# Optimization experiments

Hardware: AMD Instinct MI355X
Metric: run time of the kernel (lower is better)

The kernel has to match this reference:

```python
import jax, jax.numpy as jnp
import numpy as np

N_NODES = 40000
N_EDGES = 640000
IN_CH, HID_CH, OUT_CH = 128, 128, 64
NEG_SLOPE = 0.2  # PyG GATConv default


def _add_self_loops(src, dst, n):
    loop = jnp.arange(n, dtype=src.dtype)
    return jnp.concatenate([src, loop]), jnp.concatenate([dst, loop])


def gcn_conv(x, src, dst, W, b, n):
    # PyG GCNConv: add self-loops, symmetric degree norm, then aggregate.
    h = x @ W                                   # [N, F_out]
    s, d = _add_self_loops(src, dst, n)
    deg = jax.ops.segment_sum(jnp.ones_like(d, dtype=h.dtype), d, num_segments=n)
    dinv = jnp.where(deg > 0, jax.lax.rsqrt(deg), 0.0)
    norm = dinv[s] * dinv[d]                    # [E+N]
    msg = h[s] * norm[:, None]                  # gather + scale
    out = jax.ops.segment_sum(msg, d, num_segments=n)
    return out + b


def gat_conv(x, src, dst, W, a_src, a_dst, b, n):
    # PyG GATConv, heads=1: self-loops, edge-wise LeakyReLU attention logits,
    # softmax over incoming edges per dst node, weighted scatter-add.
    h = x @ W                                   # [N, F_out]
    s, d = _add_self_loops(src, dst, n)
    logit = jax.nn.leaky_relu((h @ a_src)[s] + (h @ a_dst)[d], NEG_SLOPE)  # [E+N]
    mx = jax.ops.segment_max(logit, d, num_segments=n)
    e = jnp.exp(logit - mx[d])
    z = jax.ops.segment_sum(e, d, num_segments=n)
    alpha = e / z[d]
    out = jax.ops.segment_sum(h[s] * alpha[:, None], d, num_segments=n)
    return out + b


def setup_inputs() -> dict:
    key = jax.random.key(0)
    ks = jax.random.split(key, 16)
    x = jax.random.normal(ks[0], (N_NODES, IN_CH), dtype=jnp.float32)
    edge_index = jax.random.randint(ks[1], (2, N_EDGES), 0, N_NODES, dtype=jnp.int64 if jax.config.jax_enable_x64 else jnp.int32)
    glorot = lambda k, fi, fo: jax.random.normal(k, (fi, fo), jnp.float32) * np.sqrt(2.0 / (fi + fo))
    params = {
        'W1': glorot(ks[2], IN_CH, HID_CH),   'b1': jnp.zeros((HID_CH,), jnp.float32),
        'Wg1': glorot(ks[3], HID_CH, HID_CH), 'ag1_src': jax.random.normal(ks[4], (HID_CH,), jnp.float32) * 0.1,
        'ag1_dst': jax.random.normal(ks[5], (HID_CH,), jnp.float32) * 0.1, 'bg1': jnp.zeros((HID_CH,), jnp.float32),
        'W2': glorot(ks[6], HID_CH, OUT_CH),  'b2': jnp.zeros((OUT_CH,), jnp.float32),
        'Wg2': glorot(ks[7], OUT_CH, OUT_CH), 'ag2_src': jax.random.normal(ks[8], (OUT_CH,), jnp.float32) * 0.1,
        'ag2_dst': jax.random.normal(ks[9], (OUT_CH,), jnp.float32) * 0.1, 'bg2': jnp.zeros((OUT_CH,), jnp.float32),
    }
    return {'x': x, 'edge_index': edge_index, **params}


def reference(x, edge_index, W1, b1, Wg1, ag1_src, ag1_dst, bg1, W2, b2, Wg2, ag2_src, ag2_dst, bg2):
    n = x.shape[0]
    src, dst = edge_index[0], edge_index[1]
    h = jax.nn.relu(gcn_conv(x, src, dst, W1, b1, n))
    # dropout(p=0.5) is identity in eval mode
    encoded = gat_conv(h, src, dst, Wg1, ag1_src, ag1_dst, bg1, n)
    h = jax.nn.relu(gcn_conv(encoded, src, dst, W2, b2, n))
    decoded = gat_conv(h, src, dst, Wg2, ag2_src, ag2_dst, bg2, n)
    return encoded, decoded
```

## Files before the change

### kernel.cpp

```cpp
#include <hip/hip_runtime.h>

#define NN 40000
#define NE 640000
#define NSB ((NN + 255) / 256)

typedef unsigned int uint32;

static __device__ __forceinline__ float lrelu(float x) { return x > 0.0f ? x : 0.2f * x; }

static __device__ __forceinline__ float wave_max(float v) {
    for (int off = 32; off; off >>= 1) v = fmaxf(v, __shfl_xor(v, off));
    return v;
}
static __device__ __forceinline__ float wave_sum(float v) {
    for (int off = 32; off; off >>= 1) v += __shfl_xor(v, off);
    return v;
}

static __device__ __forceinline__ uint32 bfr(float x) {
    uint32 u = __float_as_uint(x);
    return u + 0x7FFFu + ((u >> 16) & 1u);
}
static __device__ __forceinline__ uint32 pack2(float a, float b) {
    return (bfr(a) >> 16) | (bfr(b) & 0xFFFF0000u);
}
static __device__ __forceinline__ float lo16(uint32 v) { return __uint_as_float(v << 16); }
static __device__ __forceinline__ float hi16(uint32 v) { return __uint_as_float(v & 0xFFFF0000u); }

template <int FIN, int FOUT>
__global__ __launch_bounds__(256) void k_gemm_t(const float* __restrict__ X,
                                                const float* __restrict__ W,
                                                float* __restrict__ Y,
                                                uint32* __restrict__ Y16) {
    constexpr int XLD = FIN + 4;
    __shared__ float ws[FIN * 64];
    __shared__ float xs[64 * XLD];
    const int t = threadIdx.x;
    const int row0 = blockIdx.x * 64;
    const int col0 = blockIdx.y * 64;

    for (int i = t; i < FIN * 16; i += 256) {
        int k = i >> 4, cc = (i & 15) << 2;
        *(float4*)&ws[k * 64 + cc] = *(const float4*)&W[k * FOUT + col0 + cc];
    }
    for (int i = t; i < 64 * (FIN / 4); i += 256) {
        int r = i / (FIN / 4), kk = (i % (FIN / 4)) << 2;
        *(float4*)&xs[r * XLD + kk] = *(const float4*)&X[(size_t)(row0 + r) * FIN + kk];
    }
    __syncthreads();

    const int c0 = (t & 15) << 2;
    const int r0 = (t >> 4) << 2;
    float acc[4][4] = {};
#pragma unroll 2
    for (int k = 0; k < FIN; k += 4) {
        float4 xv[4], wv[4];
#pragma unroll
        for (int i = 0; i < 4; ++i) xv[i] = *(const float4*)&xs[(r0 + i) * XLD + k];
#pragma unroll
        for (int j = 0; j < 4; ++j) wv[j] = *(const float4*)&ws[(k + j) * 64 + c0];
#pragma unroll
        for (int i = 0; i < 4; ++i) {
            acc[i][0] = fmaf(xv[i].x, wv[0].x, acc[i][0]);
            acc[i][1] = fmaf(xv[i].x, wv[0].y, acc[i][1]);
            acc[i][2] = fmaf(xv[i].x, wv[0].z, acc[i][2]);
            acc[i][3] = fmaf(xv[i].x, wv[0].w, acc[i][3]);
            acc[i][0] = fmaf(xv[i].y, wv[1].x, acc[i][0]);
            acc[i][1] = fmaf(xv[i].y, wv[1].y, acc[i][1]);
            acc[i][2] = fmaf(xv[i].y, wv[1].z, acc[i][2]);
            acc[i][3] = fmaf(xv[i].y, wv[1].w, acc[i][3]);
            acc[i][0] = fmaf(xv[i].z, wv[2].x, acc[i][0]);
            acc[i][1] = fmaf(xv[i].z, wv[2].y, acc[i][1]);
            acc[i][2] = fmaf(xv[i].z, wv[2].z, acc[i][2]);
            acc[i][3] = fmaf(xv[i].z, wv[2].w, acc[i][3]);
            acc[i][0] = fmaf(xv[i].w, wv[3].x, acc[i][0]);
            acc[i][1] = fmaf(xv[i].w, wv[3].y, acc[i][1]);
            acc[i][2] = fmaf(xv[i].w, wv[3].z, acc[i][2]);
            acc[i][3] = fmaf(xv[i].w, wv[3].w, acc[i][3]);
        }
    }
#pragma unroll
    for (int i = 0; i < 4; ++i) {
        float4 v = make_float4(acc[i][0], acc[i][1], acc[i][2], acc[i][3]);
        size_t base = (size_t)(row0 + r0 + i) * FOUT + col0 + c0;
        *(float4*)&Y[base] = v;
        uint2 p = make_uint2(pack2(v.x, v.y), pack2(v.z, v.w));
        *(uint2*)&Y16[base >> 1] = p;
    }
}

__global__ void k_zero_int(int* __restrict__ p, int n) {
    int i = blockIdx.x * blockDim.x + threadIdx.x;
    if (i < n) p[i] = 0;
}
__global__ void k_count(const int* __restrict__ dst, int* __restrict__ cnt) {
    int e = blockIdx.x * blockDim.x + threadIdx.x;
    if (e < NE) atomicAdd(&cnt[dst[e]], 1);
}
__global__ void k_bsum(const int* __restrict__ cnt, int* __restrict__ bsum) {
    __shared__ int wsums[4];
    int i = blockIdx.x * 256 + threadIdx.x;
    int v = (i < NN) ? cnt[i] : 0;
    for (int off = 32; off; off >>= 1) v += __shfl_down(v, off);
    if ((threadIdx.x & 63) == 0) wsums[threadIdx.x >> 6] = v;
    __syncthreads();
    if (threadIdx.x == 0) bsum[blockIdx.x] = wsums[0] + wsums[1] + wsums[2] + wsums[3];
}
__global__ void k_scanpart(const int* __restrict__ bsum, int* __restrict__ bofs,
                           int* __restrict__ rowptr) {
    __shared__ int s[256];
    int t = threadIdx.x;
    int v = (t < NSB) ? bsum[t] : 0;
    s[t] = v;
    __syncthreads();
    for (int off = 1; off < 256; off <<= 1) {
        int u = (t >= off) ? s[t - off] : 0;
        __syncthreads();
        s[t] += u;
        __syncthreads();
    }
    if (t < NSB) bofs[t] = s[t] - v;
    if (t == 0) rowptr[NN] = NE;
}
__global__ void k_scatter(const int* __restrict__ cnt, const int* __restrict__ bofs,
                          int* __restrict__ rowptr, int* __restrict__ cursor) {
    __shared__ int wsums[4];
    int t = threadIdx.x;
    int lane = t & 63, w = t >> 6;
    int i = blockIdx.x * 256 + t;
    int v = (i < NN) ? cnt[i] : 0;
    int x = v;
    for (int off = 1; off < 64; off <<= 1) {
        int u = __shfl_up(x, off);
        if (lane >= off) x += u;
    }
    if (lane == 63) wsums[w] = x;
    __syncthreads();
    int wofs = 0;
    for (int k = 0; k < w; ++k) wofs += wsums[k];
    int excl = bofs[blockIdx.x] + wofs + x - v;
    if (i < NN) {
        rowptr[i] = excl;
        cursor[i] = excl;
    }
}
__global__ void k_fill(const int* __restrict__ src, const int* __restrict__ dst,
                       int* __restrict__ cursor, int* __restrict__ csr_src) {
    int e = blockIdx.x * blockDim.x + threadIdx.x;
    if (e < NE) {
        int p = atomicAdd(&cursor[dst[e]], 1);
        csr_src[p] = src[e];
    }
}
__global__ void k_dinv(const int* __restrict__ rowptr, float* __restrict__ dinv) {
    int i = blockIdx.x * blockDim.x + threadIdx.x;
    if (i < NN) dinv[i] = rsqrtf(1.0f + (float)(rowptr[i + 1] - rowptr[i]));
}

static __device__ __forceinline__ void gath128(const uint32* __restrict__ h16, int lane, int myi,
                                               float myw, int cnt, float* acc) {
    for (int j = 0; j < cnt; j += 8) {
        int s[8];
        float w[8];
#pragma unroll
        for (int u = 0; u < 8; ++u) {
            s[u] = __shfl(myi, j + u);
            w[u] = __shfl(myw, j + u);
        }
        uint32 v[8];
#pragma unroll
        for (int u = 0; u < 8; ++u) v[u] = h16[(size_t)s[u] * 64 + lane];
#pragma unroll
        for (int u = 0; u < 8; ++u) {
            acc[0] = fmaf(w[u], lo16(v[u]), acc[0]);
            acc[1] = fmaf(w[u], hi16(v[u]), acc[1]);
        }
    }
}
static __device__ __forceinline__ void gath64(const uint32* __restrict__ h16, int lane, int myi,
                                              float myw, int cnt, float* acc) {
    int hh = lane >> 5, cl = lane & 31;
    for (int j = 0; j < cnt; j += 16) {
        int s[8];
        float w[8];
#pragma unroll
        for (int u = 0; u < 8; ++u) {
            int e = j + 2 * u + hh;
            s[u] = __shfl(myi, e);
            w[u] = __shfl(myw, e);
        }
        uint32 v[8];
#pragma unroll
        for (int u = 0; u < 8; ++u) v[u] = h16[(size_t)s[u] * 32 + cl];
#pragma unroll
        for (int u = 0; u < 8; ++u) {
            acc[0] = fmaf(w[u], lo16(v[u]), acc[0]);
            acc[1] = fmaf(w[u], hi16(v[u]), acc[1]);
        }
    }
}

template <int F>
__global__ __launch_bounds__(256) void k_gcn_gather_w(const int* __restrict__ rowptr,
                                                      const int* __restrict__ csr_src,
                                                      const uint32* __restrict__ h16,
                                                      const float* __restrict__ dinv,
                                                      const float* __restrict__ b,
                                                      float* __restrict__ out) {
    int node = blockIdx.x * 4 + (threadIdx.x >> 6);
    int lane = threadIdx.x & 63;
    int beg = rowptr[node], end = rowptr[node + 1];
    float dd = dinv[node];
    float acc[2] = {0.0f, 0.0f};

    for (int g = beg; g < end; g += 64) {
        int cnt = end - g;
        if (cnt > 64) cnt = 64;
        int myi = node;
        float myw = 0.0f;
        if (lane < cnt) {
            int s = csr_src[g + lane];
            myi = s;
            myw = dinv[s];
        }
        if (F == 128)
            gath128(h16, lane, myi, myw, cnt, acc);
        else
            gath64(h16, lane, myi, myw, cnt, acc);
    }
    if (F == 128) {
        uint32 sv = h16[(size_t)node * 64 + lane];
        acc[0] = fmaf(dd, lo16(sv), acc[0]);
        acc[1] = fmaf(dd, hi16(sv), acc[1]);
        int c = lane * 2;
        float2 r;
        r.x = fmaxf(fmaf(acc[0], dd, b[c]), 0.0f);
        r.y = fmaxf(fmaf(acc[1], dd, b[c + 1]), 0.0f);
        *(float2*)&out[(size_t)node * 128 + c] = r;
    } else {
        acc[0] += __shfl_xor(acc[0], 32);
        acc[1] += __shfl_xor(acc[1], 32);
        if (lane < 32) {
            uint32 sv = h16[(size_t)node * 32 + lane];
            acc[0] = fmaf(dd, lo16(sv), acc[0]);
            acc[1] = fmaf(dd, hi16(sv), acc[1]);
            int c = lane * 2;
            float2 r;
            r.x = fmaxf(fmaf(acc[0], dd, b[c]), 0.0f);
            r.y = fmaxf(fmaf(acc[1], dd, b[c + 1]), 0.0f);
            *(float2*)&out[(size_t)node * 64 + c] = r;
        }
    }
}

__global__ void k_gat_scalars(const float* __restrict__ hg, const float* __restrict__ a_s,
                              const float* __restrict__ a_d, float* __restrict__ asrc,
                              float* __restrict__ adst, int F) {
    int node = blockIdx.x * (blockDim.x >> 6) + (threadIdx.x >> 6);
    int lane = threadIdx.x & 63;
    if (node >= NN) return;
    float s = 0.0f, d = 0.0f;
    for (int c = lane; c < F; c += 64) {
        float v = hg[(size_t)node * F + c];
        s += v * a_s[c];
        d += v * a_d[c];
    }
    for (int off = 32; off; off >>= 1) {
        s += __shfl_down(s, off);
        d += __shfl_down(d, off);
    }
    if (lane == 0) {
        asrc[node] = s;
        adst[node] = d;
    }
}

template <int F>
__global__ __launch_bounds__(256) void k_gat_gather_w(const int* __restrict__ rowptr,
                                                      const int* __restrict__ csr_src,
                                                      const uint32* __restrict__ h16,
                                                      const float* __restrict__ asrc,
                                                      const float* __restrict__ adst,
                                                      const float* __restrict__ b,
                                                      float* __restrict__ out) {
    int node = blockIdx.x * 4 + (threadIdx.x >> 6);
    int lane = threadIdx.x & 63;
    int beg = rowptr[node], end = rowptr[node + 1];
    int deg = end - beg;
    float ad = adst[node];
    float slog = lrelu(asrc[node] + ad);
    float acc[2] = {0.0f, 0.0f};
    float wself;

    if (deg <= 64) {
        int myi = node;
        float logit = -1e30f;
        if (lane < deg) {
            myi = csr_src[beg + lane];
            logit = lrelu(asrc[myi] + ad);
        }
        float m = fmaxf(slog, wave_max(logit));
        float e = (lane < deg) ? __expf(logit - m) : 0.0f;
        float z = wave_sum(e) + __expf(slog - m);
        float zi = 1.0f / z;
        float myw = e * zi;
        wself = __expf(slog - m) * zi;
        if (F == 128)
            gath128(h16, lane, myi, myw, deg, acc);
        else
            gath64(h16, lane, myi, myw, deg, acc);
    } else {
        float lm = slog;
        for (int j = beg + lane; j < end; j += 64) lm = fmaxf(lm, lrelu(asrc[csr_src[j]] + ad));
        float m = wave_max(lm);
        float lz = 0.0f;
        for (int j = beg + lane; j < end; j += 64)
            lz += __expf(lrelu(asrc[csr_src[j]] + ad) - m);
        float z = wave_sum(lz) + __expf(slog - m);
        float zi = 1.0f / z;
        wself = __expf(slog - m) * zi;
        for (int g = beg; g < end; g += 64) {
            int cnt = end - g;
            if (cnt > 64) cnt = 64;
            int myi = node;
            float myw = 0.0f;
            if (lane < cnt) {
                int s = csr_src[g + lane];
                myi = s;
                myw = __expf(lrelu(asrc[s] + ad) - m) * zi;
            }
            if (F == 128)
                gath128(h16, lane, myi, myw, cnt, acc);
            else
                gath64(h16, lane, myi, myw, cnt, acc);
        }
    }
    if (F == 128) {
        uint32 sv = h16[(size_t)node * 64 + lane];
        acc[0] = fmaf(wself, lo16(sv), acc[0]);
        acc[1] = fmaf(wself, hi16(sv), acc[1]);
        int c = lane * 2;
        float2 r;
        r.x = acc[0] + b[c];
        r.y = acc[1] + b[c + 1];
        *(float2*)&out[(size_t)node * 128 + c] = r;
    } else {
        acc[0] += __shfl_xor(acc[0], 32);
        acc[1] += __shfl_xor(acc[1], 32);
        if (lane < 32) {
            uint32 sv = h16[(size_t)node * 32 + lane];
            acc[0] = fmaf(wself, lo16(sv), acc[0]);
            acc[1] = fmaf(wself, hi16(sv), acc[1]);
            int c = lane * 2;
            float2 r;
            r.x = acc[0] + b[c];
            r.y = acc[1] + b[c + 1];
            *(float2*)&out[(size_t)node * 64 + c] = r;
        }
    }
}

extern "C" void kernel_launch(void* const* d_in, const int* in_sizes, int n_in,
                              void* d_out, int out_size, void* d_ws, size_t ws_size,
                              hipStream_t stream) {
    const float* x = (const float*)d_in[0];
    const int* src = (const int*)d_in[1];
    const int* dst = src + NE;
    const float* W1 = (const float*)d_in[2];
    const float* b1 = (const float*)d_in[3];
    const float* Wg1 = (const float*)d_in[4];
    const float* ag1s = (const float*)d_in[5];
    const float* ag1d = (const float*)d_in[6];
    const float* bg1 = (const float*)d_in[7];
    const float* W2 = (const float*)d_in[8];
    const float* b2 = (const float*)d_in[9];
    const float* Wg2 = (const float*)d_in[10];
    const float* ag2s = (const float*)d_in[11];
    const float* ag2d = (const float*)d_in[12];
    const float* bg2 = (const float*)d_in[13];

    float* enc = (float*)d_out;
    float* dec = enc + (size_t)NN * 128;

    float* ws = (float*)d_ws;
    float* bufA = ws;
    float* bufB = bufA + (size_t)NN * 128;
    uint32* bufA16 = (uint32*)(bufB + (size_t)NN * 128);
    float* dinv = (float*)(bufA16 + (size_t)NN * 64);
    float* asrc = dinv + NN;
    float* adst = asrc + NN;
    int* cnt = (int*)(adst + NN);
    int* rowptr = cnt + NN;
    int* cursor = rowptr + NN + 1;
    int* csr_src = cursor + NN;
    int* bsum = csr_src + NE;
    int* bofs = bsum + NSB;

    const int TB = 256;
    int gN = (NN + TB - 1) / TB;
    int gE = (NE + TB - 1) / TB;
    int gScal = (NN + 3) / 4;
    int gWave = NN / 4;

    k_zero_int<<<gN, TB, 0, stream>>>(cnt, NN);
    k_count<<<gE, TB, 0, stream>>>(dst, cnt);
    k_bsum<<<NSB, 256, 0, stream>>>(cnt, bsum);
    k_scanpart<<<1, 256, 0, stream>>>(bsum, bofs, rowptr);
    k_scatter<<<NSB, 256, 0, stream>>>(cnt, bofs, rowptr, cursor);
    k_fill<<<gE, TB, 0, stream>>>(src, dst, cursor, csr_src);
    k_dinv<<<gN, TB, 0, stream>>>(rowptr, dinv);

    k_gemm_t<128, 128><<<dim3(NN / 64, 2), 256, 0, stream>>>(x, W1, bufA, bufA16);
    k_gcn_gather_w<128><<<gWave, 256, 0, stream>>>(rowptr, csr_src, bufA16, dinv, b1, bufB);

    k_gemm_t<128, 128><<<dim3(NN / 64, 2), 256, 0, stream>>>(bufB, Wg1, bufA, bufA16);
    k_gat_scalars<<<gScal, TB, 0, stream>>>(bufA, ag1s, ag1d, asrc, adst, 128);
    k_gat_gather_w<128><<<gWave, 256, 0, stream>>>(rowptr, csr_src, bufA16, asrc, adst, bg1, enc);

    k_gemm_t<128, 64><<<dim3(NN / 64, 1), 256, 0, stream>>>(enc, W2, bufA, bufA16);
    k_gcn_gather_w<64><<<gWave, 256, 0, stream>>>(rowptr, csr_src, bufA16, dinv, b2, bufB);

    k_gemm_t<64, 64><<<dim3(NN / 64, 1), 256, 0, stream>>>(bufB, Wg2, bufA, bufA16);
    k_gat_scalars<<<gScal, TB, 0, stream>>>(bufA, ag2s, ag2d, asrc, adst, 64);
    k_gat_gather_w<64><<<gWave, 256, 0, stream>>>(rowptr, csr_src, bufA16, asrc, adst, bg2, dec);
}
```

Measured before the change: 264.1 us.

## Use bf16 MFMA GEMMs with bf16 intermediate activations between layers

```diff
diff --git a/kernel.cpp b/kernel.cpp
--- a/kernel.cpp
+++ b/kernel.cpp
@@ -3,8 +3,12 @@
 #define NN 40000
 #define NE 640000
 #define NSB ((NN + 255) / 256)
+#define NNP (NN + 64)
 
 typedef unsigned int uint32;
+typedef unsigned short ushort;
+typedef __attribute__((ext_vector_type(8))) short bf16x8;
+typedef __attribute__((ext_vector_type(4))) float f32x4;
 
 static __device__ __forceinline__ float lrelu(float x) { return x > 0.0f ? x : 0.2f * x; }
 
@@ -21,72 +25,96 @@
     uint32 u = __float_as_uint(x);
     return u + 0x7FFFu + ((u >> 16) & 1u);
 }
+static __device__ __forceinline__ ushort bf16of(float x) { return (ushort)(bfr(x) >> 16); }
 static __device__ __forceinline__ uint32 pack2(float a, float b) {
     return (bfr(a) >> 16) | (bfr(b) & 0xFFFF0000u);
 }
 static __device__ __forceinline__ float lo16(uint32 v) { return __uint_as_float(v << 16); }
 static __device__ __forceinline__ float hi16(uint32 v) { return __uint_as_float(v & 0xFFFF0000u); }
 
-template <int FIN, int FOUT>
-__global__ __launch_bounds__(256) void k_gemm_t(const float* __restrict__ X,
-                                                const float* __restrict__ W,
-                                                float* __restrict__ Y,
-                                                uint32* __restrict__ Y16) {
-    constexpr int XLD = FIN + 4;
-    __shared__ float ws[FIN * 64];
-    __shared__ float xs[64 * XLD];
-    const int t = threadIdx.x;
-    const int row0 = blockIdx.x * 64;
-    const int col0 = blockIdx.y * 64;
-
-    for (int i = t; i < FIN * 16; i += 256) {
-        int k = i >> 4, cc = (i & 15) << 2;
-        *(float4*)&ws[k * 64 + cc] = *(const float4*)&W[k * FOUT + col0 + cc];
-    }
-    for (int i = t; i < 64 * (FIN / 4); i += 256) {
-        int r = i / (FIN / 4), kk = (i % (FIN / 4)) << 2;
-        *(float4*)&xs[r * XLD + kk] = *(const float4*)&X[(size_t)(row0 + r) * FIN + kk];
-    }
-    __syncthreads();
-
-    const int c0 = (t & 15) << 2;
-    const int r0 = (t >> 4) << 2;
-    float acc[4][4] = {};
-#pragma unroll 2
-    for (int k = 0; k < FIN; k += 4) {
-        float4 xv[4], wv[4];
-#pragma unroll
-        for (int i = 0; i < 4; ++i) xv[i] = *(const float4*)&xs[(r0 + i) * XLD + k];
-#pragma unroll
-        for (int j = 0; j < 4; ++j) wv[j] = *(const float4*)&ws[(k + j) * 64 + c0];
-#pragma unroll
-        for (int i = 0; i < 4; ++i) {
-            acc[i][0] = fmaf(xv[i].x, wv[0].x, acc[i][0]);
-            acc[i][1] = fmaf(xv[i].x, wv[0].y, acc[i][1]);
-            acc[i][2] = fmaf(xv[i].x, wv[0].z, acc[i][2]);
-            acc[i][3] = fmaf(xv[i].x, wv[0].w, acc[i][3]);
-            acc[i][0] = fmaf(xv[i].y, wv[1].x, acc[i][0]);
-            acc[i][1] = fmaf(xv[i].y, wv[1].y, acc[i][1]);
-            acc[i][2] = fmaf(xv[i].y, wv[1].z, acc[i][2]);
-            acc[i][3] = fmaf(xv[i].y, wv[1].w, acc[i][3]);
-            acc[i][0] = fmaf(xv[i].z, wv[2].x, acc[i][0]);
-            acc[i][1] = fmaf(xv[i].z, wv[2].y, acc[i][1]);
-            acc[i][2] = fmaf(xv[i].z, wv[2].z, acc[i][2]);
-            acc[i][3] = fmaf(xv[i].z, wv[2].w, acc[i][3]);
-            acc[i][0] = fmaf(xv[i].w, wv[3].x, acc[i][0]);
-            acc[i][1] = fmaf(xv[i].w, wv[3].y, acc[i][1]);
-            acc[i][2] = fmaf(xv[i].w, wv[3].z, acc[i][2]);
-            acc[i][3] = fmaf(xv[i].w, wv[3].w, acc[i][3]);
-        }
-    }
-#pragma unroll
-    for (int i = 0; i < 4; ++i) {
-        float4 v = make_float4(acc[i][0], acc[i][1], acc[i][2], acc[i][3]);
-        size_t base = (size_t)(row0 + r0 + i) * FOUT + col0 + c0;
-        *(float4*)&Y[base] = v;
-        uint2 p = make_uint2(pack2(v.x, v.y), pack2(v.z, v.w));
-        *(uint2*)&Y16[base >> 1] = p;
-    }
+__global__ void k_xcast(const float* __restrict__ x, ushort* __restrict__ xb) {
+    int i = blockIdx.x * blockDim.x + threadIdx.x;
+    int base = i * 4;
+    if (base < NN * 128) {
+        float4 v = *(const float4*)&x[base];
+        ushort4 o;
+        o.x = bf16of(v.x);
+        o.y = bf16of(v.y);
+        o.z = bf16of(v.z);
+        o.w = bf16of(v.w);
+        *(ushort4*)&xb[base] = o;
+    }
+}
+__global__ void k_wcast(const float* __restrict__ W1, const float* __restrict__ Wg1,
+                        const float* __restrict__ W2, const float* __restrict__ Wg2,
+                        ushort* __restrict__ t1, ushort* __restrict__ tg1,
+                        ushort* __restrict__ t2, ushort* __restrict__ tg2) {
+    const float* W;
+    ushort* T;
+    int K, N;
+    switch (blockIdx.y) {
+        case 0: W = W1; T = t1; K = 128; N = 128; break;
+        case 1: W = Wg1; T = tg1; K = 128; N = 128; break;
+        case 2: W = W2; T = t2; K = 128; N = 64; break;
+        default: W = Wg2; T = tg2; K = 64; N = 64; break;
+    }
+    int idx = blockIdx.x * 256 + threadIdx.x;
+    if (idx < K * N) {
+        int n = idx / K, k = idx % K;
+        T[idx] = bf16of(W[k * N + n]);
+    }
+}
+
+template <int FIN, int FOUT, bool WF32>
+__global__ __launch_bounds__(256) void k_gemm_mfma(const ushort* __restrict__ Xb,
+                                                   const ushort* __restrict__ Wt,
+                                                   float* __restrict__ Y,
+                                                   ushort* __restrict__ Y16) {
+    constexpr int NT = FOUT / 16;
+    const int w = threadIdx.x >> 6, lane = threadIdx.x & 63;
+    const int row0 = blockIdx.x * 128 + w * 32;
+    const int lr = lane & 15;
+    const int lk = (lane >> 4) * 8;
+
+    f32x4 acc[2][NT];
+#pragma unroll
+    for (int mt = 0; mt < 2; ++mt)
+#pragma unroll
+        for (int nt = 0; nt < NT; ++nt) acc[mt][nt] = (f32x4){0.f, 0.f, 0.f, 0.f};
+
+#pragma unroll
+    for (int ks = 0; ks < FIN / 32; ++ks) {
+        bf16x8 a[2], b[NT];
+#pragma unroll
+        for (int mt = 0; mt < 2; ++mt)
+            a[mt] = *(const bf16x8*)&Xb[(size_t)(row0 + mt * 16 + lr) * FIN + ks * 32 + lk];
+#pragma unroll
+        for (int nt = 0; nt < NT; ++nt)
+            b[nt] = *(const bf16x8*)&Wt[(size_t)(nt * 16 + lr) * FIN + ks * 32 + lk];
+#pragma unroll
+        for (int mt = 0; mt < 2; ++mt)
+#pragma unroll
+            for (int nt = 0; nt < NT; ++nt)
+                acc[mt][nt] =
+                    __builtin_amdgcn_mfma_f32_16x16x32_bf16(a[mt], b[nt], acc[mt][nt], 0, 0, 0);
+    }
+
+    const int rbase = (lane >> 4) * 4;
+#pragma unroll
+    for (int mt = 0; mt < 2; ++mt)
+#pragma unroll
+        for (int nt = 0; nt < NT; ++nt) {
+            int col = nt * 16 + lr;
+#pragma unroll
+            for (int i = 0; i < 4; ++i) {
+                int r = row0 + mt * 16 + rbase + i;
+                if (r < NN) {
+                    float v = acc[mt][nt][i];
+                    if (WF32) Y[(size_t)r * FOUT + col] = v;
+                    Y16[(size_t)r * FOUT + col] = bf16of(v);
+                }
+            }
+        }
 }
 
 __global__ void k_zero_int(int* __restrict__ p, int n) {
@@ -123,7 +151,8 @@
     if (t == 0) rowptr[NN] = NE;
 }
 __global__ void k_scatter(const int* __restrict__ cnt, const int* __restrict__ bofs,
-                          int* __restrict__ rowptr, int* __restrict__ cursor) {
+                          int* __restrict__ rowptr, int* __restrict__ cursor,
+                          float* __restrict__ dinv) {
     __shared__ int wsums[4];
     int t = threadIdx.x;
     int lane = t & 63, w = t >> 6;
@@ -142,6 +171,7 @@
     if (i < NN) {
         rowptr[i] = excl;
         cursor[i] = excl;
+        dinv[i] = rsqrtf(1.0f + (float)v);
     }
 }
 __global__ void k_fill(const int* __restrict__ src, const int* __restrict__ dst,
@@ -152,10 +182,6 @@
         csr_src[p] = src[e];
     }
 }
-__global__ void k_dinv(const int* __restrict__ rowptr, float* __restrict__ dinv) {
-    int i = blockIdx.x * blockDim.x + threadIdx.x;
-    if (i < NN) dinv[i] = rsqrtf(1.0f + (float)(rowptr[i + 1] - rowptr[i]));
-}
 
 static __device__ __forceinline__ void gath128(const uint32* __restrict__ h16, int lane, int myi,
                                                float myw, int cnt, float* acc) {
@@ -206,7 +232,7 @@
                                                       const uint32* __restrict__ h16,
                                                       const float* __restrict__ dinv,
                                                       const float* __restrict__ b,
-                                                      float* __restrict__ out) {
+                                                      uint32* __restrict__ out16) {
     int node = blockIdx.x * 4 + (threadIdx.x >> 6);
     int lane = threadIdx.x & 63;
     int beg = rowptr[node], end = rowptr[node + 1];
@@ -233,10 +259,9 @@
         acc[0] = fmaf(dd, lo16(sv), acc[0]);
         acc[1] = fmaf(dd, hi16(sv), acc[1]);
         int c = lane * 2;
-        float2 r;
-        r.x = fmaxf(fmaf(acc[0], dd, b[c]), 0.0f);
-        r.y = fmaxf(fmaf(acc[1], dd, b[c + 1]), 0.0f);
-        *(float2*)&out[(size_t)node * 128 + c] = r;
+        float rx = fmaxf(fmaf(acc[0], dd, b[c]), 0.0f);
+        float ry = fmaxf(fmaf(acc[1], dd, b[c + 1]), 0.0f);
+        out16[(size_t)node * 64 + lane] = pack2(rx, ry);
     } else {
         acc[0] += __shfl_xor(acc[0], 32);
         acc[1] += __shfl_xor(acc[1], 32);
@@ -245,10 +270,9 @@
             acc[0] = fmaf(dd, lo16(sv), acc[0]);
             acc[1] = fmaf(dd, hi16(sv), acc[1]);
             int c = lane * 2;
-            float2 r;
-            r.x = fmaxf(fmaf(acc[0], dd, b[c]), 0.0f);
-            r.y = fmaxf(fmaf(acc[1], dd, b[c + 1]), 0.0f);
-            *(float2*)&out[(size_t)node * 64 + c] = r;
+            float rx = fmaxf(fmaf(acc[0], dd, b[c]), 0.0f);
+            float ry = fmaxf(fmaf(acc[1], dd, b[c + 1]), 0.0f);
+            out16[(size_t)node * 32 + lane] = pack2(rx, ry);
         }
     }
 }
@@ -275,14 +299,15 @@
     }
 }
 
-template <int F>
+template <int F, bool WB16>
 __global__ __launch_bounds__(256) void k_gat_gather_w(const int* __restrict__ rowptr,
                                                       const int* __restrict__ csr_src,
                                                       const uint32* __restrict__ h16,
                                                       const float* __restrict__ asrc,
                                                       const float* __restrict__ adst,
                                                       const float* __restrict__ b,
-                                                      float* __restrict__ out) {
+                                                      float* __restrict__ out,
+                                                      uint32* __restrict__ out16) {
     int node = blockIdx.x * 4 + (threadIdx.x >> 6);
     int lane = threadIdx.x & 63;
     int beg = rowptr[node], end = rowptr[node + 1];
@@ -344,6 +369,7 @@
         r.x = acc[0] + b[c];
         r.y = acc[1] + b[c + 1];
         *(float2*)&out[(size_t)node * 128 + c] = r;
+        if (WB16) out16[(size_t)node * 64 + lane] = pack2(r.x, r.y);
     } else {
         acc[0] += __shfl_xor(acc[0], 32);
         acc[1] += __shfl_xor(acc[1], 32);
@@ -356,6 +382,7 @@
             r.x = acc[0] + b[c];
             r.y = acc[1] + b[c + 1];
             *(float2*)&out[(size_t)node * 64 + c] = r;
+            if (WB16) out16[(size_t)node * 32 + lane] = pack2(r.x, r.y);
         }
     }
 }
@@ -382,11 +409,16 @@
     float* enc = (float*)d_out;
     float* dec = enc + (size_t)NN * 128;
 
-    float* ws = (float*)d_ws;
-    float* bufA = ws;
-    float* bufB = bufA + (size_t)NN * 128;
-    uint32* bufA16 = (uint32*)(bufB + (size_t)NN * 128);
-    float* dinv = (float*)(bufA16 + (size_t)NN * 64);
+    float* bufA = (float*)d_ws;
+    ushort* ush = (ushort*)(bufA + (size_t)NN * 128);
+    ushort* m0 = ush;
+    ushort* m1 = m0 + (size_t)NNP * 128;
+    ushort* m2 = m1 + (size_t)NNP * 128;
+    ushort* wt1 = m2 + (size_t)NNP * 128;
+    ushort* wtg1 = wt1 + 128 * 128;
+    ushort* wt2 = wtg1 + 128 * 128;
+    ushort* wtg2 = wt2 + 64 * 128;
+    float* dinv = (float*)(wtg2 + 64 * 64);
     float* asrc = dinv + NN;
     float* adst = asrc + NN;
     int* cnt = (int*)(adst + NN);
@@ -401,26 +433,33 @@
     int gE = (NE + TB - 1) / TB;
     int gScal = (NN + 3) / 4;
     int gWave = NN / 4;
+    int gM = (NN + 127) / 128;
+
+    k_xcast<<<(NN * 128 / 4 + TB - 1) / TB, TB, 0, stream>>>(x, m0);
+    k_wcast<<<dim3(64, 4), TB, 0, stream>>>(W1, Wg1, W2, Wg2, wt1, wtg1, wt2, wtg2);
 
     k_zero_int<<<gN, TB, 0, stream>>>(cnt, NN);
     k_count<<<gE, TB, 0, stream>>>(dst, cnt);
     k_bsum<<<NSB, 256, 0, stream>>>(cnt, bsum);
     k_scanpart<<<1, 256, 0, stream>>>(bsum, bofs, rowptr);
-    k_scatter<<<NSB, 256, 0, stream>>>(cnt, bofs, rowptr, cursor);
+    k_scatter<<<NSB, 256, 0, stream>>>(cnt, bofs, rowptr, cursor, dinv);
     k_fill<<<gE, TB, 0, stream>>>(src, dst, cursor, csr_src);
-    k_dinv<<<gN, TB, 0, stream>>>(rowptr, dinv);
-
-    k_gemm_t<128, 128><<<dim3(NN / 64, 2), 256, 0, stream>>>(x, W1, bufA, bufA16);
-    k_gcn_gather_w<128><<<gWave, 256, 0, stream>>>(rowptr, csr_src, bufA16, dinv, b1, bufB);
-
-    k_gemm_t<128, 128><<<dim3(NN / 64, 2), 256, 0, stream>>>(bufB, Wg1, bufA, bufA16);
+
+    k_gemm_mfma<128, 128, false><<<gM, 256, 0, stream>>>(m0, wt1, bufA, m2);
+    k_gcn_gather_w<128><<<gWave, 256, 0, stream>>>(rowptr, csr_src, (uint32*)m2, dinv, b1,
+                                                   (uint32*)m1);
+
+    k_gemm_mfma<128, 128, true><<<gM, 256, 0, stream>>>(m1, wtg1, bufA, m2);
     k_gat_scalars<<<gScal, TB, 0, stream>>>(bufA, ag1s, ag1d, asrc, adst, 128);
-    k_gat_gather_w<128><<<gWave, 256, 0, stream>>>(rowptr, csr_src, bufA16, asrc, adst, bg1, enc);
-
-    k_gemm_t<128, 64><<<dim3(NN / 64, 1), 256, 0, stream>>>(enc, W2, bufA, bufA16);
-    k_gcn_gather_w<64><<<gWave, 256, 0, stream>>>(rowptr, csr_src, bufA16, dinv, b2, bufB);
-
-    k_gemm_t<64, 64><<<dim3(NN / 64, 1), 256, 0, stream>>>(bufB, Wg2, bufA, bufA16);
+    k_gat_gather_w<128, true><<<gWave, 256, 0, stream>>>(rowptr, csr_src, (uint32*)m2, asrc,
+                                                         adst, bg1, enc, (uint32*)m0);
+
+    k_gemm_mfma<128, 64, false><<<gM, 256, 0, stream>>>(m0, wt2, bufA, m2);
+    k_gcn_gather_w<64><<<gWave, 256, 0, stream>>>(rowptr, csr_src, (uint32*)m2, dinv, b2,
+                                                  (uint32*)m1);
+
+    k_gemm_mfma<64, 64, true><<<gM, 256, 0, stream>>>(m1, wtg2, bufA, m2);
     k_gat_scalars<<<gScal, TB, 0, stream>>>(bufA, ag2s, ag2d, asrc, adst, 64);
-    k_gat_gather_w<64><<<gWave, 256, 0, stream>>>(rowptr, csr_src, bufA16, asrc, adst, bg2, dec);
-}
+    k_gat_gather_w<64, false><<<gWave, 256, 0, stream>>>(rowptr, csr_src, (uint32*)m2, asrc,
+                                                         adst, bg2, dec, (uint32*)m0);
+}
```

Measured after the change: 241.2 us. 8.7% less time.
